# Kernel tuning notes

Hardware: AMD Instinct MI355X
Metric: run time of the kernel (lower is better)

Reference implementation:

```python
import jax, jax.numpy as jnp
import numpy as np

N = 131072
N_DIM = 128
NUM_LAYERS = 8
N_MID = NUM_LAYERS - 2  # middle (n_dim -> n_dim) layers


def _sigmoid_layer(h, u_un, w_un, log_a, b):
    # h: [N, in]; u_un: [out, in]; w_un: [out, out]; log_a, b: [out, 1]
    a = jnp.exp(log_a)                      # [out, 1]
    u = jax.nn.softmax(u_un, axis=1)        # row-softmax, matches Softmax(dim=1)
    w = jax.nn.softmax(w_un, axis=1)
    inner = h @ (a * u).T + b[:, 0]         # [N, out]
    return jax.nn.sigmoid(inner) @ w.T      # [N, out]


def setup_inputs() -> dict:
    key = jax.random.key(0)
    ks = jax.random.split(key, 24)
    d = N_DIM
    inp = {
        "x": jax.random.normal(ks[0], (N,), jnp.float32),
        "fy0": jax.random.normal(ks[1], (N,), jnp.float32),
        # first layer (in=2, out=d)
        "u0": jax.random.normal(ks[2], (d, 2), jnp.float32),
        "w0": jax.random.normal(ks[3], (d, d), jnp.float32),
        "la0": jax.random.normal(ks[4], (d, 1), jnp.float32),
        "b0": jax.random.normal(ks[5], (d, 1), jnp.float32),
        # middle layers stacked (in=d, out=d)
        "uM": jax.random.normal(ks[6], (N_MID, d, d), jnp.float32),
        "wM": jax.random.normal(ks[7], (N_MID, d, d), jnp.float32),
        "laM": jax.random.normal(ks[8], (N_MID, d, 1), jnp.float32),
        "bM": jax.random.normal(ks[9], (N_MID, d, 1), jnp.float32),
        # last layer (in=d, out=1)
        "uL": jax.random.normal(ks[10], (1, d), jnp.float32),
        "wL": jax.random.normal(ks[11], (1, 1), jnp.float32),
        "laL": jax.random.normal(ks[12], (1, 1), jnp.float32),
        "bL": jax.random.normal(ks[13], (1, 1), jnp.float32),
        # MLP 1 -> 50 -> 50 -> 1
        "W1": jax.random.normal(ks[14], (50, 1), jnp.float32) * 0.2,
        "b1": jax.random.normal(ks[15], (50,), jnp.float32) * 0.2,
        "W2": jax.random.normal(ks[16], (50, 50), jnp.float32) * 0.1,
        "b2": jax.random.normal(ks[17], (50,), jnp.float32) * 0.1,
        "W3": jax.random.normal(ks[18], (1, 50), jnp.float32) * 0.1,
        "b3": jax.random.normal(ks[19], (1,), jnp.float32) * 0.1,
    }
    return inp


def reference(x, fy0, u0, w0, la0, b0, uM, wM, laM, bM, uL, wL, laL, bL,
              W1, b1, W2, b2, W3, b3):
    # MLP feature net on fy0: [N,1] -> [N,1]
    h = jax.nn.relu(fy0[:, None] @ W1.T + b1)
    h = jax.nn.relu(h @ W2.T + b2)
    theta = h @ W3.T + b3                          # [N, 1]
    mono = jnp.concatenate([x[:, None], theta], 1)  # [N, 2]

    mono = _sigmoid_layer(mono, u0, w0, la0, b0)    # [N, d]

    def step(carry, p):
        u_un, w_un, log_a, b = p
        return _sigmoid_layer(carry, u_un, w_un, log_a, b), None

    mono, _ = jax.lax.scan(step, mono, (uM, wM, laM, bM))
    out = _sigmoid_layer(mono, uL, wL, laL, bL)     # [N, 1]
    return out[:, :, None]                          # [N, 1, 1] matches torch
```

## Files before the change

kernel.cpp:

```cpp
#include <hip/hip_runtime.h>
#include <cstdint>

typedef __attribute__((ext_vector_type(8))) _Float16 half8;
typedef __attribute__((ext_vector_type(4))) _Float16 half4;
typedef __attribute__((ext_vector_type(2))) _Float16 half2v;
typedef __attribute__((ext_vector_type(16))) float f32x16;
typedef __attribute__((ext_vector_type(4))) float f4;

#define LOG2E 1.44269504088896340f
#define KNL  (-1.44269504088896340f)

__device__ __forceinline__ float fast_exp(float x) { return __builtin_amdgcn_exp2f(LOG2E * x); }
__device__ __forceinline__ float sigmoidf(float v) {
    return __builtin_amdgcn_rcpf(1.f + __builtin_amdgcn_exp2f(KNL * v));
}
__device__ __forceinline__ float sig2(float y) {
    return __builtin_amdgcn_rcpf(1.f + __builtin_amdgcn_exp2f(y));
}
__device__ __forceinline__ unsigned pk2(float a, float b) {
    half2v h = { (_Float16)a, (_Float16)b };
    return __builtin_bit_cast(unsigned, h);
}
__device__ __forceinline__ void swapl(unsigned& a, unsigned& b) {
    asm volatile("v_permlane32_swap_b32 %0, %1" : "+v"(a), "+v"(b));
}
__device__ __forceinline__ void swaplf(float& a, float& b) {
    asm volatile("v_permlane32_swap_b32 %0, %1" : "+v"(a), "+v"(b));
}
union BU { unsigned u[4]; half8 h; };

constexpr int A0X = 0, A0T = 128, B0O = 256, BMO = 384, VLO = 1152,
              W1P = 1280, B1P = 1344, B2P = 1408, W3P = 1472, CN = 1536;

constexpr int GHIO  = 0;
constexpr int GLOO  = 6 * 32768;
constexpr int W2HIO = 12 * 32768;
constexpr int W2LOO = W2HIO + 8192;
constexpr int CGOFF = W2LOO + 8192;

__global__ __launch_bounds__(256)
void prep_kernel(const float* __restrict__ u0, const float* __restrict__ w0,
                 const float* __restrict__ la0, const float* __restrict__ b0,
                 const float* __restrict__ uM, const float* __restrict__ wM,
                 const float* __restrict__ laM, const float* __restrict__ bM,
                 const float* __restrict__ uL, const float* __restrict__ laL,
                 const float* __restrict__ W1, const float* __restrict__ b1,
                 const float* __restrict__ W2, const float* __restrict__ b2,
                 const float* __restrict__ W3,
                 char* __restrict__ Ghi, char* __restrict__ Glo,
                 _Float16* __restrict__ W2hi, _Float16* __restrict__ W2lo,
                 float* __restrict__ CgF)
{
    __shared__ float Wl[128 * 136];
    __shared__ float Al[8 * 132];
    __shared__ float uls[128];

    const int tid = threadIdx.x, b = blockIdx.x;
    const bool mblk = (b < 96);
    const int l = mblk ? (b >> 4) : 6;

    {
        const float* Wsrc = (l == 0) ? w0 : wM + (l - 1) * 16384;
        const int r = tid >> 1, h = tid & 1;
        const float* rp = Wsrc + r * 128 + h * 64;
        f4 buf[16];
#pragma unroll
        for (int v = 0; v < 16; ++v) buf[v] = *(const f4*)(rp + 4 * v);
        float mx = -1e30f;
#pragma unroll
        for (int v = 0; v < 16; ++v)
#pragma unroll
            for (int e = 0; e < 4; ++e) mx = fmaxf(mx, buf[v][e]);
        mx = fmaxf(mx, __shfl_xor(mx, 1));
        float s = 0.f;
#pragma unroll
        for (int v = 0; v < 16; ++v)
#pragma unroll
            for (int e = 0; e < 4; ++e) { buf[v][e] = fast_exp(buf[v][e] - mx); s += buf[v][e]; }
        s += __shfl_xor(s, 1);
        float inv = 1.f / s;
#pragma unroll
        for (int v = 0; v < 16; ++v)
            *(f4*)(&Wl[r * 136 + h * 64 + 4 * v]) = buf[v] * inv;
    }

    if (mblk) {
        const int q = b & 15;
        const int rl = tid >> 5, part = tid & 31;
        const int gi = q * 8 + rl;
        {
            f4 ub = *(const f4*)(uM + (l * 128 + gi) * 128 + part * 4);
            float mx = fmaxf(fmaxf(ub[0], ub[1]), fmaxf(ub[2], ub[3]));
#pragma unroll
            for (int o = 1; o < 32; o <<= 1) mx = fmaxf(mx, __shfl_xor(mx, o));
            float s = 0.f;
#pragma unroll
            for (int e = 0; e < 4; ++e) { ub[e] = fast_exp(ub[e] - mx); s += ub[e]; }
#pragma unroll
            for (int o = 1; o < 32; o <<= 1) s += __shfl_xor(s, o);
            float sc = fast_exp(laM[l * 128 + gi]) / s;
            *(f4*)(&Al[rl * 132 + part * 4]) = ub * sc;
        }
        __syncthreads();
        const int j0 = part * 4;
        f4 acc = {};
        for (int k = 0; k < 128; ++k) {
            float a = Al[rl * 132 + k];
            acc += a * *(const f4*)(&Wl[k * 136 + j0]);
        }
        const int sw = (gi & 15) << 4;
        char* bh = Ghi + l * 32768 + gi * 256;
        char* bl = Glo + l * 32768 + gi * 256;
        half4 hv, lv;
#pragma unroll
        for (int e = 0; e < 4; ++e) {
            float m = KNL * acc[e];
            _Float16 hh = (_Float16)m;
            hv[e] = hh;
            lv[e] = (_Float16)(m - (float)hh);
        }
        *(half4*)(bh + ((2 * j0) ^ sw)) = hv;
        *(half4*)(bl + 2 * j0) = lv;
    } else {
        if (tid < 64) {
            float v0 = uL[tid], v1 = uL[tid + 64];
            float mx = fmaxf(v0, v1);
#pragma unroll
            for (int o = 32; o; o >>= 1) mx = fmaxf(mx, __shfl_xor(mx, o));
            float e0 = fast_exp(v0 - mx), e1 = fast_exp(v1 - mx);
            float ssum = e0 + e1;
#pragma unroll
            for (int o = 32; o; o >>= 1) ssum += __shfl_xor(ssum, o);
            float aL = fast_exp(laL[0]) / ssum;
            uls[tid]      = e0 * aL;
            uls[tid + 64] = e1 * aL;
        }
        __syncthreads();
        if (tid < 128) {
            float s = 0.f;
            for (int k = 0; k < 128; ++k) s += uls[k] * Wl[k * 136 + tid];
            CgF[VLO + tid] = s;
        }
        if (tid < 128) {
            const int j = tid;
            float q0 = u0[2 * j], q1 = u0[2 * j + 1];
            float mx = fmaxf(q0, q1);
            float e0 = fast_exp(q0 - mx), e1 = fast_exp(q1 - mx);
            float a = fast_exp(la0[j]) / (e0 + e1);
            CgF[A0X + j] = KNL * a * e0;
            CgF[A0T + j] = KNL * a * e1;
            CgF[B0O + j] = KNL * b0[j];
        } else if (tid < 192) {
            const int t = tid - 128;
            CgF[W1P + t] = (t < 50) ? W1[t] : 0.f;
            CgF[B1P + t] = (t < 50) ? b1[t] : 0.f;
            CgF[B2P + t] = (t < 50) ? b2[t] : 0.f;
            CgF[W3P + t] = (t < 50) ? W3[t] : 0.f;
        }
        for (int i = tid; i < 768; i += 256) CgF[BMO + i] = KNL * bM[i];
        for (int i = tid; i < 4096; i += 256) {
            int r = i >> 6, c = i & 63;
            float v = (r < 50 && c < 50) ? W2[r * 50 + c] : 0.f;
            _Float16 h = (_Float16)v;
            W2hi[i] = h;
            W2lo[i] = (_Float16)(v - (float)h);
        }
    }
}


__device__ __forceinline__ void stage32(char* ls, const char* gs, int tid) {
#pragma unroll
    for (int i = 0; i < 8; ++i)
        __builtin_amdgcn_global_load_lds(
            (const __attribute__((address_space(1))) unsigned*)(uintptr_t)(gs + tid * 16 + i * 4096),
            (__attribute__((address_space(3))) unsigned*)(uintptr_t)(ls + tid * 16 + i * 4096),
            16, 0, 0);
}

__device__ __forceinline__ void epi_nt(const f32x16& a0, const f32x16& a1,
                                       half8& o00, half8& o01, half8& o10, half8& o11)
{
#pragma unroll
    for (int bt = 0; bt < 2; ++bt) {
        const f32x16& A = bt ? a1 : a0;
        unsigned p00 = pk2(sig2(A[0]),  sig2(A[1]));
        unsigned p01 = pk2(sig2(A[2]),  sig2(A[3]));
        unsigned p10 = pk2(sig2(A[4]),  sig2(A[5]));
        unsigned p11 = pk2(sig2(A[6]),  sig2(A[7]));
        unsigned p20 = pk2(sig2(A[8]),  sig2(A[9]));
        unsigned p21 = pk2(sig2(A[10]), sig2(A[11]));
        unsigned p30 = pk2(sig2(A[12]), sig2(A[13]));
        unsigned p31 = pk2(sig2(A[14]), sig2(A[15]));
        swapl(p00, p10); swapl(p01, p11);
        swapl(p20, p30); swapl(p21, p31);
        BU u0; u0.u[0] = p00; u0.u[1] = p01; u0.u[2] = p10; u0.u[3] = p11;
        BU u1; u1.u[0] = p20; u1.u[1] = p21; u1.u[2] = p30; u1.u[3] = p31;
        if (bt == 0) { o00 = u0.h; o01 = u1.h; }
        else         { o10 = u0.h; o11 = u1.h; }
    }
}

__device__ __forceinline__ void do_layer(const char* bufHi, const char* gLo,
                                         const half8 (&Bin)[2][8], half8 (&Bout)[2][8],
                                         const float* __restrict__ biasK,
                                         int l31, int hi)
{
    const int sw = (l31 & 15) << 4;
#pragma unroll
    for (int nt = 0; nt < 4; ++nt) {
        f4 bv0 = *(const f4*)(biasK + 32 * nt + 4 * hi);
        f4 bv1 = *(const f4*)(biasK + 32 * nt + 8 + 4 * hi);
        f4 bv2 = *(const f4*)(biasK + 32 * nt + 16 + 4 * hi);
        f4 bv3 = *(const f4*)(biasK + 32 * nt + 24 + 4 * hi);
        f32x16 a0 = { bv0[0], bv0[1], bv0[2], bv0[3],
                      bv1[0], bv1[1], bv1[2], bv1[3],
                      bv2[0], bv2[1], bv2[2], bv2[3],
                      bv3[0], bv3[1], bv3[2], bv3[3] };
        f32x16 a1 = a0;
        const char* rhi = bufHi + (nt * 32 + l31) * 256;
        const char* rlo = gLo + (nt * 32 + l31) * 256;
#pragma unroll
        for (int ks = 0; ks < 8; ++ks) {
            half8 Ah = *(const half8*)(rhi + ((ks * 32 + hi * 16) ^ sw));
            half8 Al = *(const half8*)(rlo + ks * 32 + hi * 16);
            a0 = __builtin_amdgcn_mfma_f32_32x32x16_f16(Ah, Bin[0][ks], a0, 0, 0, 0);
            a1 = __builtin_amdgcn_mfma_f32_32x32x16_f16(Ah, Bin[1][ks], a1, 0, 0, 0);
            a0 = __builtin_amdgcn_mfma_f32_32x32x16_f16(Al, Bin[0][ks], a0, 0, 0, 0);
            a1 = __builtin_amdgcn_mfma_f32_32x32x16_f16(Al, Bin[1][ks], a1, 0, 0, 0);
        }
        epi_nt(a0, a1, Bout[0][2 * nt], Bout[0][2 * nt + 1],
               Bout[1][2 * nt], Bout[1][2 * nt + 1]);
    }
}

__global__ __launch_bounds__(256, 2)
void mono_main(const float* __restrict__ x, const float* __restrict__ fy0,
               const char* __restrict__ Ghi, const char* __restrict__ Glo,
               const _Float16* __restrict__ W2hi, const _Float16* __restrict__ W2lo,
               const float* __restrict__ CgF, const float* __restrict__ b3g,
               const float* __restrict__ bLg, float* __restrict__ out)
{
    extern __shared__ __align__(16) char sm[];
    char* buf0 = sm;
    char* buf1 = sm + 32768;

    const int tid = threadIdx.x;
    const int lane = tid & 63, wave = tid >> 6;
    const int l31 = lane & 31, hi = lane >> 5;
    const int row0 = blockIdx.x * 256 + wave * 64;

    stage32(buf0, Ghi, tid);
    const float b3s = b3g[0], bLs = bLg[0];

    float fy[2] = { fy0[row0 + l31], fy0[row0 + 32 + l31] };
    half8 Bm[2][4];
#pragma unroll
    for (int ks = 0; ks < 4; ++ks) {
        f4 w1a = *(const f4*)(CgF + W1P + 16 * ks + 8 * hi);
        f4 w1b = *(const f4*)(CgF + W1P + 16 * ks + 8 * hi + 4);
        f4 b1a = *(const f4*)(CgF + B1P + 16 * ks + 8 * hi);
        f4 b1b = *(const f4*)(CgF + B1P + 16 * ks + 8 * hi + 4);
#pragma unroll
        for (int bt = 0; bt < 2; ++bt) {
            BU u;
            u.u[0] = pk2(fmaxf(fy[bt] * w1a[0] + b1a[0], 0.f), fmaxf(fy[bt] * w1a[1] + b1a[1], 0.f));
            u.u[1] = pk2(fmaxf(fy[bt] * w1a[2] + b1a[2], 0.f), fmaxf(fy[bt] * w1a[3] + b1a[3], 0.f));
            u.u[2] = pk2(fmaxf(fy[bt] * w1b[0] + b1b[0], 0.f), fmaxf(fy[bt] * w1b[1] + b1b[1], 0.f));
            u.u[3] = pk2(fmaxf(fy[bt] * w1b[2] + b1b[2], 0.f), fmaxf(fy[bt] * w1b[3] + b1b[3], 0.f));
            Bm[bt][ks] = u.h;
        }
    }

    f32x16 a00 = {}, a01 = {}, a10 = {}, a11 = {};
#pragma unroll
    for (int nt = 0; nt < 2; ++nt)
#pragma unroll
        for (int ks = 0; ks < 4; ++ks) {
            half8 Ah = *(const half8*)(W2hi + (nt * 32 + l31) * 64 + ks * 16 + hi * 8);
            half8 Al = *(const half8*)(W2lo + (nt * 32 + l31) * 64 + ks * 16 + hi * 8);
            if (nt == 0) {
                a00 = __builtin_amdgcn_mfma_f32_32x32x16_f16(Ah, Bm[0][ks], a00, 0, 0, 0);
                a10 = __builtin_amdgcn_mfma_f32_32x32x16_f16(Ah, Bm[1][ks], a10, 0, 0, 0);
                a00 = __builtin_amdgcn_mfma_f32_32x32x16_f16(Al, Bm[0][ks], a00, 0, 0, 0);
                a10 = __builtin_amdgcn_mfma_f32_32x32x16_f16(Al, Bm[1][ks], a10, 0, 0, 0);
            } else {
                a01 = __builtin_amdgcn_mfma_f32_32x32x16_f16(Ah, Bm[0][ks], a01, 0, 0, 0);
                a11 = __builtin_amdgcn_mfma_f32_32x32x16_f16(Ah, Bm[1][ks], a11, 0, 0, 0);
                a01 = __builtin_amdgcn_mfma_f32_32x32x16_f16(Al, Bm[0][ks], a01, 0, 0, 0);
                a11 = __builtin_amdgcn_mfma_f32_32x32x16_f16(Al, Bm[1][ks], a11, 0, 0, 0);
            }
        }

    float tp0 = 0.f, tp1 = 0.f;
#pragma unroll
    for (int nt = 0; nt < 2; ++nt)
#pragma unroll
        for (int g = 0; g < 4; ++g) {
            f4 w3 = *(const f4*)(CgF + W3P + 32 * nt + 8 * g + 4 * hi);
            f4 b2v = *(const f4*)(CgF + B2P + 32 * nt + 8 * g + 4 * hi);
            const f32x16& A0 = nt ? a01 : a00;
            const f32x16& A1 = nt ? a11 : a10;
#pragma unroll
            for (int e = 0; e < 4; ++e) {
                tp0 += w3[e] * fmaxf(A0[4 * g + e] + b2v[e], 0.f);
                tp1 += w3[e] * fmaxf(A1[4 * g + e] + b2v[e], 0.f);
            }
        }
    swaplf(tp0, tp1);
    float th = tp0 + tp1 + b3s;
    float t0 = th, t1 = th;
    swaplf(t0, t1);

    float xr[2] = { x[row0 + l31], x[row0 + 32 + l31] };
    float thv[2] = { t0, t1 };
    half8 Bq[2][8], Bp[2][8];
#pragma unroll
    for (int ks = 0; ks < 8; ++ks) {
        f4 axa = *(const f4*)(CgF + A0X + 16 * ks + 8 * hi);
        f4 axb = *(const f4*)(CgF + A0X + 16 * ks + 8 * hi + 4);
        f4 ata = *(const f4*)(CgF + A0T + 16 * ks + 8 * hi);
        f4 atb = *(const f4*)(CgF + A0T + 16 * ks + 8 * hi + 4);
        f4 b0a = *(const f4*)(CgF + B0O + 16 * ks + 8 * hi);
        f4 b0b = *(const f4*)(CgF + B0O + 16 * ks + 8 * hi + 4);
#pragma unroll
        for (int bt = 0; bt < 2; ++bt) {
            BU u;
            u.u[0] = pk2(sig2(axa[0] * xr[bt] + ata[0] * thv[bt] + b0a[0]),
                         sig2(axa[1] * xr[bt] + ata[1] * thv[bt] + b0a[1]));
            u.u[1] = pk2(sig2(axa[2] * xr[bt] + ata[2] * thv[bt] + b0a[2]),
                         sig2(axa[3] * xr[bt] + ata[3] * thv[bt] + b0a[3]));
            u.u[2] = pk2(sig2(axb[0] * xr[bt] + atb[0] * thv[bt] + b0b[0]),
                         sig2(axb[1] * xr[bt] + atb[1] * thv[bt] + b0b[1]));
            u.u[3] = pk2(sig2(axb[2] * xr[bt] + atb[2] * thv[bt] + b0b[2]),
                         sig2(axb[3] * xr[bt] + atb[3] * thv[bt] + b0b[3]));
            Bq[bt][ks] = u.h;
        }
    }
    __syncthreads();

    stage32(buf1, Ghi + 1 * 32768, tid);
    do_layer(buf0, Glo + 0 * 32768, Bq, Bp, CgF + BMO + 0 * 128, l31, hi);
    __syncthreads();
    stage32(buf0, Ghi + 2 * 32768, tid);
    do_layer(buf1, Glo + 1 * 32768, Bp, Bq, CgF + BMO + 1 * 128, l31, hi);
    __syncthreads();
    stage32(buf1, Ghi + 3 * 32768, tid);
    do_layer(buf0, Glo + 2 * 32768, Bq, Bp, CgF + BMO + 2 * 128, l31, hi);
    __syncthreads();
    stage32(buf0, Ghi + 4 * 32768, tid);
    do_layer(buf1, Glo + 3 * 32768, Bp, Bq, CgF + BMO + 3 * 128, l31, hi);
    __syncthreads();
    stage32(buf1, Ghi + 5 * 32768, tid);
    do_layer(buf0, Glo + 4 * 32768, Bq, Bp, CgF + BMO + 4 * 128, l31, hi);
    __syncthreads();
    do_layer(buf1, Glo + 5 * 32768, Bp, Bq, CgF + BMO + 5 * 128, l31, hi);

    float d0 = 0.f, d1 = 0.f;
#pragma unroll
    for (int ks = 0; ks < 8; ++ks) {
        f4 va = *(const f4*)(CgF + VLO + 16 * ks + 8 * hi);
        f4 vb = *(const f4*)(CgF + VLO + 16 * ks + 8 * hi + 4);
        half8 s0 = Bq[0][ks], s1 = Bq[1][ks];
#pragma unroll
        for (int e = 0; e < 4; ++e) {
            d0 += va[e] * (float)s0[e] + vb[e] * (float)s0[e + 4];
            d1 += va[e] * (float)s1[e] + vb[e] * (float)s1[e + 4];
        }
    }
    swaplf(d0, d1);
    out[row0 + lane] = sigmoidf(d0 + d1 + bLs);
}

extern "C" void kernel_launch(void* const* d_in, const int* in_sizes, int n_in,
                              void* d_out, int out_size, void* d_ws, size_t ws_size,
                              hipStream_t stream)
{
    const float* x   = (const float*)d_in[0];
    const float* fy0 = (const float*)d_in[1];
    const float* u0  = (const float*)d_in[2];
    const float* w0  = (const float*)d_in[3];
    const float* la0 = (const float*)d_in[4];
    const float* b0  = (const float*)d_in[5];
    const float* uM  = (const float*)d_in[6];
    const float* wM  = (const float*)d_in[7];
    const float* laM = (const float*)d_in[8];
    const float* bM  = (const float*)d_in[9];
    const float* uL  = (const float*)d_in[10];
    const float* laL = (const float*)d_in[12];
    const float* bL  = (const float*)d_in[13];
    const float* W1  = (const float*)d_in[14];
    const float* b1  = (const float*)d_in[15];
    const float* W2  = (const float*)d_in[16];
    const float* b2  = (const float*)d_in[17];
    const float* W3  = (const float*)d_in[18];
    const float* b3  = (const float*)d_in[19];
    float* out = (float*)d_out;

    char* ws = (char*)d_ws;
    char*     Ghi  = ws + GHIO;
    char*     Glo  = ws + GLOO;
    _Float16* W2hi = (_Float16*)(ws + W2HIO);
    _Float16* W2lo = (_Float16*)(ws + W2LOO);
    float*    CgF  = (float*)(ws + CGOFF);

    prep_kernel<<<97, 256, 0, stream>>>(u0, w0, la0, b0, uM, wM, laM, bM,
                                        uL, laL, W1, b1, W2, b2, W3,
                                        Ghi, Glo, W2hi, W2lo, CgF);

    static bool attr_set = false;
    if (!attr_set) {
        hipFuncSetAttribute((const void*)mono_main,
                            hipFuncAttributeMaxDynamicSharedMemorySize, 65536);
        attr_set = true;
    }
    mono_main<<<512, 256, 65536, stream>>>(x, fy0, Ghi, Glo, W2hi, W2lo,
                                           CgF, b3, bL, out);
}
```

Measured before the change: 169.0 us.

## Stage both hi and lo weight halves into LDS, single-buffered per layer

Previously only the high half of each layer's split-fp16 weight matrix was staged into LDS (double-buffered), while the low half was read straight from global memory. Now prep packs hi and lo together into one 64KB block per layer, stages the whole block into LDS with a single buffer, and reads both halves from LDS using the same swizzle. The cost is losing the overlap of the next layer's load with the current layer's compute, since staging now sits between barriers. It also splits the MFMA accumulation into even and odd chains to shorten dependencies, raises wave priority around the MFMA loop, and switches fp16 packing to the cvt_pkrtz builtin (round-toward-zero).

After: 160.3 us. 5.1% less time.

```diff
diff --git a/kernel.cpp b/kernel.cpp
--- a/kernel.cpp
+++ b/kernel.cpp
@@ -17,9 +17,8 @@
 __device__ __forceinline__ float sig2(float y) {
     return __builtin_amdgcn_rcpf(1.f + __builtin_amdgcn_exp2f(y));
 }
-__device__ __forceinline__ unsigned pk2(float a, float b) {
-    half2v h = { (_Float16)a, (_Float16)b };
-    return __builtin_bit_cast(unsigned, h);
+__device__ __forceinline__ unsigned pkz(float a, float b) {
+    return __builtin_bit_cast(unsigned, __builtin_amdgcn_cvt_pkrtz(a, b));
 }
 __device__ __forceinline__ void swapl(unsigned& a, unsigned& b) {
     asm volatile("v_permlane32_swap_b32 %0, %1" : "+v"(a), "+v"(b));
@@ -32,9 +31,8 @@
 constexpr int A0X = 0, A0T = 128, B0O = 256, BMO = 384, VLO = 1152,
               W1P = 1280, B1P = 1344, B2P = 1408, W3P = 1472, CN = 1536;
 
-constexpr int GHIO  = 0;
-constexpr int GLOO  = 6 * 32768;
-constexpr int W2HIO = 12 * 32768;
+constexpr int GOFF  = 0;
+constexpr int W2HIO = 6 * 65536;
 constexpr int W2LOO = W2HIO + 8192;
 constexpr int CGOFF = W2LOO + 8192;
 
@@ -47,9 +45,8 @@
                  const float* __restrict__ W1, const float* __restrict__ b1,
                  const float* __restrict__ W2, const float* __restrict__ b2,
                  const float* __restrict__ W3,
-                 char* __restrict__ Ghi, char* __restrict__ Glo,
-                 _Float16* __restrict__ W2hi, _Float16* __restrict__ W2lo,
-                 float* __restrict__ CgF)
+                 char* __restrict__ G, _Float16* __restrict__ W2hi,
+                 _Float16* __restrict__ W2lo, float* __restrict__ CgF)
 {
     __shared__ float Wl[128 * 136];
     __shared__ float Al[8 * 132];
@@ -102,15 +99,15 @@
             *(f4*)(&Al[rl * 132 + part * 4]) = ub * sc;
         }
         __syncthreads();
-        const int j0 = part * 4;
+        const int j0 = (tid & 31) * 4;
         f4 acc = {};
         for (int k = 0; k < 128; ++k) {
             float a = Al[rl * 132 + k];
             acc += a * *(const f4*)(&Wl[k * 136 + j0]);
         }
-        const int sw = (gi & 15) << 4;
-        char* bh = Ghi + l * 32768 + gi * 256;
-        char* bl = Glo + l * 32768 + gi * 256;
+        const int sw = (gi & 7) << 4;
+        char* bh = G + l * 65536 + gi * 256;
+        char* bl = bh + 32768;
         half4 hv, lv;
 #pragma unroll
         for (int e = 0; e < 4; ++e) {
@@ -120,7 +117,7 @@
             lv[e] = (_Float16)(m - (float)hh);
         }
         *(half4*)(bh + ((2 * j0) ^ sw)) = hv;
-        *(half4*)(bl + 2 * j0) = lv;
+        *(half4*)(bl + ((2 * j0) ^ sw)) = lv;
     } else {
         if (tid < 64) {
             float v0 = uL[tid], v1 = uL[tid + 64];
@@ -169,9 +166,9 @@
 }
 
 
-__device__ __forceinline__ void stage32(char* ls, const char* gs, int tid) {
-#pragma unroll
-    for (int i = 0; i < 8; ++i)
+__device__ __forceinline__ void stage64(char* ls, const char* gs, int tid) {
+#pragma unroll
+    for (int i = 0; i < 16; ++i)
         __builtin_amdgcn_global_load_lds(
             (const __attribute__((address_space(1))) unsigned*)(uintptr_t)(gs + tid * 16 + i * 4096),
             (__attribute__((address_space(3))) unsigned*)(uintptr_t)(ls + tid * 16 + i * 4096),
@@ -184,14 +181,14 @@
 #pragma unroll
     for (int bt = 0; bt < 2; ++bt) {
         const f32x16& A = bt ? a1 : a0;
-        unsigned p00 = pk2(sig2(A[0]),  sig2(A[1]));
-        unsigned p01 = pk2(sig2(A[2]),  sig2(A[3]));
-        unsigned p10 = pk2(sig2(A[4]),  sig2(A[5]));
-        unsigned p11 = pk2(sig2(A[6]),  sig2(A[7]));
-        unsigned p20 = pk2(sig2(A[8]),  sig2(A[9]));
-        unsigned p21 = pk2(sig2(A[10]), sig2(A[11]));
-        unsigned p30 = pk2(sig2(A[12]), sig2(A[13]));
-        unsigned p31 = pk2(sig2(A[14]), sig2(A[15]));
+        unsigned p00 = pkz(sig2(A[0]),  sig2(A[1]));
+        unsigned p01 = pkz(sig2(A[2]),  sig2(A[3]));
+        unsigned p10 = pkz(sig2(A[4]),  sig2(A[5]));
+        unsigned p11 = pkz(sig2(A[6]),  sig2(A[7]));
+        unsigned p20 = pkz(sig2(A[8]),  sig2(A[9]));
+        unsigned p21 = pkz(sig2(A[10]), sig2(A[11]));
+        unsigned p30 = pkz(sig2(A[12]), sig2(A[13]));
+        unsigned p31 = pkz(sig2(A[14]), sig2(A[15]));
         swapl(p00, p10); swapl(p01, p11);
         swapl(p20, p30); swapl(p21, p31);
         BU u0; u0.u[0] = p00; u0.u[1] = p01; u0.u[2] = p10; u0.u[3] = p11;
@@ -201,34 +198,46 @@
     }
 }
 
-__device__ __forceinline__ void do_layer(const char* bufHi, const char* gLo,
+__device__ __forceinline__ void do_layer(const char* buf,
                                          const half8 (&Bin)[2][8], half8 (&Bout)[2][8],
                                          const float* __restrict__ biasK,
                                          int l31, int hi)
 {
-    const int sw = (l31 & 15) << 4;
+    const int sw = (l31 & 7) << 4;
 #pragma unroll
     for (int nt = 0; nt < 4; ++nt) {
         f4 bv0 = *(const f4*)(biasK + 32 * nt + 4 * hi);
         f4 bv1 = *(const f4*)(biasK + 32 * nt + 8 + 4 * hi);
         f4 bv2 = *(const f4*)(biasK + 32 * nt + 16 + 4 * hi);
         f4 bv3 = *(const f4*)(biasK + 32 * nt + 24 + 4 * hi);
-        f32x16 a0 = { bv0[0], bv0[1], bv0[2], bv0[3],
-                      bv1[0], bv1[1], bv1[2], bv1[3],
-                      bv2[0], bv2[1], bv2[2], bv2[3],
-                      bv3[0], bv3[1], bv3[2], bv3[3] };
-        f32x16 a1 = a0;
-        const char* rhi = bufHi + (nt * 32 + l31) * 256;
-        const char* rlo = gLo + (nt * 32 + l31) * 256;
-#pragma unroll
-        for (int ks = 0; ks < 8; ++ks) {
-            half8 Ah = *(const half8*)(rhi + ((ks * 32 + hi * 16) ^ sw));
-            half8 Al = *(const half8*)(rlo + ks * 32 + hi * 16);
-            a0 = __builtin_amdgcn_mfma_f32_32x32x16_f16(Ah, Bin[0][ks], a0, 0, 0, 0);
-            a1 = __builtin_amdgcn_mfma_f32_32x32x16_f16(Ah, Bin[1][ks], a1, 0, 0, 0);
-            a0 = __builtin_amdgcn_mfma_f32_32x32x16_f16(Al, Bin[0][ks], a0, 0, 0, 0);
-            a1 = __builtin_amdgcn_mfma_f32_32x32x16_f16(Al, Bin[1][ks], a1, 0, 0, 0);
-        }
+        f32x16 a0e = { bv0[0], bv0[1], bv0[2], bv0[3],
+                       bv1[0], bv1[1], bv1[2], bv1[3],
+                       bv2[0], bv2[1], bv2[2], bv2[3],
+                       bv3[0], bv3[1], bv3[2], bv3[3] };
+        f32x16 a1e = a0e;
+        f32x16 a0o = {}, a1o = {};
+        const char* rhi = buf + (nt * 32 + l31) * 256;
+        const char* rlo = rhi + 32768;
+        __builtin_amdgcn_s_setprio(1);
+#pragma unroll
+        for (int ks = 0; ks < 8; ks += 2) {
+            const int offE = (ks * 32 + hi * 16) ^ sw;
+            const int offO = ((ks + 1) * 32 + hi * 16) ^ sw;
+            half8 AhE = *(const half8*)(rhi + offE);
+            half8 AhO = *(const half8*)(rhi + offO);
+            half8 AlE = *(const half8*)(rlo + offE);
+            half8 AlO = *(const half8*)(rlo + offO);
+            a0e = __builtin_amdgcn_mfma_f32_32x32x16_f16(AhE, Bin[0][ks],     a0e, 0, 0, 0);
+            a1e = __builtin_amdgcn_mfma_f32_32x32x16_f16(AhE, Bin[1][ks],     a1e, 0, 0, 0);
+            a0o = __builtin_amdgcn_mfma_f32_32x32x16_f16(AhO, Bin[0][ks + 1], a0o, 0, 0, 0);
+            a1o = __builtin_amdgcn_mfma_f32_32x32x16_f16(AhO, Bin[1][ks + 1], a1o, 0, 0, 0);
+            a0e = __builtin_amdgcn_mfma_f32_32x32x16_f16(AlE, Bin[0][ks],     a0e, 0, 0, 0);
+            a1e = __builtin_amdgcn_mfma_f32_32x32x16_f16(AlE, Bin[1][ks],     a1e, 0, 0, 0);
+            a0o = __builtin_amdgcn_mfma_f32_32x32x16_f16(AlO, Bin[0][ks + 1], a0o, 0, 0, 0);
+            a1o = __builtin_amdgcn_mfma_f32_32x32x16_f16(AlO, Bin[1][ks + 1], a1o, 0, 0, 0);
+        }
+        __builtin_amdgcn_s_setprio(0);
+        f32x16 a0 = a0e + a0o, a1 = a1e + a1o;
         epi_nt(a0, a1, Bout[0][2 * nt], Bout[0][2 * nt + 1],
                Bout[1][2 * nt], Bout[1][2 * nt + 1]);
     }
@@ -236,21 +245,19 @@
 
 __global__ __launch_bounds__(256, 2)
 void mono_main(const float* __restrict__ x, const float* __restrict__ fy0,
-               const char* __restrict__ Ghi, const char* __restrict__ Glo,
+               const char* __restrict__ G,
                const _Float16* __restrict__ W2hi, const _Float16* __restrict__ W2lo,
                const float* __restrict__ CgF, const float* __restrict__ b3g,
                const float* __restrict__ bLg, float* __restrict__ out)
 {
     extern __shared__ __align__(16) char sm[];
-    char* buf0 = sm;
-    char* buf1 = sm + 32768;
 
     const int tid = threadIdx.x;
     const int lane = tid & 63, wave = tid >> 6;
     const int l31 = lane & 31, hi = lane >> 5;
     const int row0 = blockIdx.x * 256 + wave * 64;
 
-    stage32(buf0, Ghi, tid);
+    stage64(sm, G, tid);
     const float b3s = b3g[0], bLs = bLg[0];
 
     float fy[2] = { fy0[row0 + l31], fy0[row0 + 32 + l31] };
@@ -264,10 +271,10 @@
 #pragma unroll
         for (int bt = 0; bt < 2; ++bt) {
             BU u;
-            u.u[0] = pk2(fmaxf(fy[bt] * w1a[0] + b1a[0], 0.f), fmaxf(fy[bt] * w1a[1] + b1a[1], 0.f));
-            u.u[1] = pk2(fmaxf(fy[bt] * w1a[2] + b1a[2], 0.f), fmaxf(fy[bt] * w1a[3] + b1a[3], 0.f));
-            u.u[2] = pk2(fmaxf(fy[bt] * w1b[0] + b1b[0], 0.f), fmaxf(fy[bt] * w1b[1] + b1b[1], 0.f));
-            u.u[3] = pk2(fmaxf(fy[bt] * w1b[2] + b1b[2], 0.f), fmaxf(fy[bt] * w1b[3] + b1b[3], 0.f));
+            u.u[0] = pkz(fmaxf(fy[bt] * w1a[0] + b1a[0], 0.f), fmaxf(fy[bt] * w1a[1] + b1a[1], 0.f));
+            u.u[1] = pkz(fmaxf(fy[bt] * w1a[2] + b1a[2], 0.f), fmaxf(fy[bt] * w1a[3] + b1a[3], 0.f));
+            u.u[2] = pkz(fmaxf(fy[bt] * w1b[0] + b1b[0], 0.f), fmaxf(fy[bt] * w1b[1] + b1b[1], 0.f));
+            u.u[3] = pkz(fmaxf(fy[bt] * w1b[2] + b1b[2], 0.f), fmaxf(fy[bt] * w1b[3] + b1b[3], 0.f));
             Bm[bt][ks] = u.h;
         }
     }
@@ -326,35 +333,40 @@
 #pragma unroll
         for (int bt = 0; bt < 2; ++bt) {
             BU u;
-            u.u[0] = pk2(sig2(axa[0] * xr[bt] + ata[0] * thv[bt] + b0a[0]),
+            u.u[0] = pkz(sig2(axa[0] * xr[bt] + ata[0] * thv[bt] + b0a[0]),
                          sig2(axa[1] * xr[bt] + ata[1] * thv[bt] + b0a[1]));
-            u.u[1] = pk2(sig2(axa[2] * xr[bt] + ata[2] * thv[bt] + b0a[2]),
+            u.u[1] = pkz(sig2(axa[2] * xr[bt] + ata[2] * thv[bt] + b0a[2]),
                          sig2(axa[3] * xr[bt] + ata[3] * thv[bt] + b0a[3]));
-            u.u[2] = pk2(sig2(axb[0] * xr[bt] + atb[0] * thv[bt] + b0b[0]),
+            u.u[2] = pkz(sig2(axb[0] * xr[bt] + atb[0] * thv[bt] + b0b[0]),
                          sig2(axb[1] * xr[bt] + atb[1] * thv[bt] + b0b[1]));
-            u.u[3] = pk2(sig2(axb[2] * xr[bt] + atb[2] * thv[bt] + b0b[2]),
+            u.u[3] = pkz(sig2(axb[2] * xr[bt] + atb[2] * thv[bt] + b0b[2]),
                          sig2(axb[3] * xr[bt] + atb[3] * thv[bt] + b0b[3]));
             Bq[bt][ks] = u.h;
         }
     }
     __syncthreads();
 
-    stage32(buf1, Ghi + 1 * 32768, tid);
-    do_layer(buf0, Glo + 0 * 32768, Bq, Bp, CgF + BMO + 0 * 128, l31, hi);
-    __syncthreads();
-    stage32(buf0, Ghi + 2 * 32768, tid);
-    do_layer(buf1, Glo + 1 * 32768, Bp, Bq, CgF + BMO + 1 * 128, l31, hi);
-    __syncthreads();
-    stage32(buf1, Ghi + 3 * 32768, tid);
-    do_layer(buf0, Glo + 2 * 32768, Bq, Bp, CgF + BMO + 2 * 128, l31, hi);
-    __syncthreads();
-    stage32(buf0, Ghi + 4 * 32768, tid);
-    do_layer(buf1, Glo + 3 * 32768, Bp, Bq, CgF + BMO + 3 * 128, l31, hi);
-    __syncthreads();
-    stage32(buf1, Ghi + 5 * 32768, tid);
-    do_layer(buf0, Glo + 4 * 32768, Bq, Bp, CgF + BMO + 4 * 128, l31, hi);
-    __syncthreads();
-    do_layer(buf1, Glo + 5 * 32768, Bp, Bq, CgF + BMO + 5 * 128, l31, hi);
+    do_layer(sm, Bq, Bp, CgF + BMO + 0 * 128, l31, hi);
+    __syncthreads();
+    stage64(sm, G + 1 * 65536, tid);
+    __syncthreads();
+    do_layer(sm, Bp, Bq, CgF + BMO + 1 * 128, l31, hi);
+    __syncthreads();
+    stage64(sm, G + 2 * 65536, tid);
+    __syncthreads();
+    do_layer(sm, Bq, Bp, CgF + BMO + 2 * 128, l31, hi);
+    __syncthreads();
+    stage64(sm, G + 3 * 65536, tid);
+    __syncthreads();
+    do_layer(sm, Bp, Bq, CgF + BMO + 3 * 128, l31, hi);
+    __syncthreads();
+    stage64(sm, G + 4 * 65536, tid);
+    __syncthreads();
+    do_layer(sm, Bq, Bp, CgF + BMO + 4 * 128, l31, hi);
+    __syncthreads();
+    stage64(sm, G + 5 * 65536, tid);
+    __syncthreads();
+    do_layer(sm, Bp, Bq, CgF + BMO + 5 * 128, l31, hi);
 
     float d0 = 0.f, d1 = 0.f;
 #pragma unroll
@@ -398,15 +410,14 @@
     float* out = (float*)d_out;
 
     char* ws = (char*)d_ws;
-    char*     Ghi  = ws + GHIO;
-    char*     Glo  = ws + GLOO;
+    char*     Gz   = ws + GOFF;
     _Float16* W2hi = (_Float16*)(ws + W2HIO);
     _Float16* W2lo = (_Float16*)(ws + W2LOO);
     float*    CgF  = (float*)(ws + CGOFF);
 
     prep_kernel<<<97, 256, 0, stream>>>(u0, w0, la0, b0, uM, wM, laM, bM,
                                         uL, laL, W1, b1, W2, b2, W3,
-                                        Ghi, Glo, W2hi, W2lo, CgF);
+                                        Gz, W2hi, W2lo, CgF);
 
     static bool attr_set = false;
     if (!attr_set) {
@@ -414,6 +425,6 @@
                             hipFuncAttributeMaxDynamicSharedMemorySize, 65536);
         attr_set = true;
     }
-    mono_main<<<512, 256, 65536, stream>>>(x, fy0, Ghi, Glo, W2hi, W2lo,
+    mono_main<<<512, 256, 65536, stream>>>(x, fy0, Gz, W2hi, W2lo,
                                            CgF, b3, bL, out);
 }
```
